# Kernel optimization log

Hardware: AMD Instinct MI355X
Metric: run time of the kernel (lower is better)

## Reference

```python
import jax, jax.numpy as jnp
import numpy as np

B, T, D = 4, 4096, 1024
H, HD = 16, 64
EPS = 1e-6


def setup_inputs() -> dict:
    key = jax.random.key(0)
    ks = jax.random.split(key, 5)
    scale = 1.0 / np.sqrt(D)
    return {
        "x": jax.random.normal(ks[0], (B, T, D), dtype=jnp.float32),
        "Wq": jax.random.normal(ks[1], (D, H * HD), dtype=jnp.float32) * scale,
        "Wk": jax.random.normal(ks[2], (D, H * HD), dtype=jnp.float32) * scale,
        "Wv": jax.random.normal(ks[3], (D, H * HD), dtype=jnp.float32) * scale,
        "Wo": jax.random.normal(ks[4], (H * HD, D), dtype=jnp.float32) * scale,
    }


def _feature_map(x):
    # ELU + 1 feature map (always positive)
    return jax.nn.elu(x) + 1.0


def _causal_linear_attention(q, k, v, eps=EPS):
    # q,k,v: (B,H,T,Dk/Dv) -> scan over T with running state
    Dk = q.shape[-1]
    Dv = v.shape[-1]
    qT = jnp.moveaxis(q, 2, 0)  # (T,B,H,Dk)
    kT = jnp.moveaxis(k, 2, 0)
    vT = jnp.moveaxis(v, 2, 0)

    S0 = jnp.zeros((q.shape[0], q.shape[1], Dk, Dv), dtype=q.dtype)
    z0 = jnp.zeros((q.shape[0], q.shape[1], Dk), dtype=q.dtype)

    def step(carry, qkv_t):
        S, z = carry
        q_t, k_t, v_t = qkv_t
        S = S + jnp.einsum('bhd,bhe->bhde', k_t, v_t)
        z = z + k_t
        num = jnp.einsum('bhd,bhde->bhe', q_t, S)
        den = jnp.einsum('bhd,bhd->bh', q_t, z) + eps
        return (S, z), num / den[..., None]

    _, yT = jax.lax.scan(step, (S0, z0), (qT, kT, vT))  # yT: (T,B,H,Dv)
    return jnp.moveaxis(yT, 0, 2)  # (B,H,T,Dv)


def reference(x, Wq, Wk, Wv, Wo):
    b, t, _ = x.shape

    def proj(W):
        return (x @ W).reshape(b, t, H, HD).transpose(0, 2, 1, 3)  # (B,H,T,HD)

    q = _feature_map(proj(Wq))
    k = _feature_map(proj(Wk))
    v = proj(Wv)
    y = _causal_linear_attention(q, k, v)  # (B,H,T,HD)
    y = y.transpose(0, 2, 1, 3).reshape(b, t, H * HD)
    return y @ Wo
```

## Files before the change

kernel.cpp:

```cpp
#include <hip/hip_runtime.h>


typedef __bf16 bf16;
typedef __bf16 bf16x4 __attribute__((ext_vector_type(4)));
typedef __bf16 bf16x8 __attribute__((ext_vector_type(8)));
typedef float f32x4 __attribute__((ext_vector_type(4)));

#define EPS 1e-6f

#define BAR() asm volatile("s_barrier" ::: "memory")
#define VMCNT4() asm volatile("s_waitcnt vmcnt(4)" ::: "memory")
#define VMCNT0() asm volatile("s_waitcnt vmcnt(0)" ::: "memory")

__device__ __forceinline__ void gl_lds16(const void* g, void* l) {
  __builtin_amdgcn_global_load_lds(
      (__attribute__((address_space(1))) void*)g,
      (__attribute__((address_space(3))) void*)l, 16, 0, 0);
}

__device__ __forceinline__ float fmact(float v) {
  return v > 0.f ? v + 1.f : __expf(v);
}

__global__ __launch_bounds__(256) void cvt_bf16(const float* __restrict__ in,
                                                bf16* __restrict__ out, int n8) {
  int i = blockIdx.x * 256 + threadIdx.x;
  if (i >= n8) return;
  size_t base = (size_t)i * 8;
  float4 v0 = *(const float4*)&in[base];
  float4 v1 = *(const float4*)&in[base + 4];
  bf16x8 o;
  o[0] = (bf16)v0.x; o[1] = (bf16)v0.y; o[2] = (bf16)v0.z; o[3] = (bf16)v0.w;
  o[4] = (bf16)v1.x; o[5] = (bf16)v1.y; o[6] = (bf16)v1.z; o[7] = (bf16)v1.w;
  *(bf16x8*)&out[base] = o;
}

__global__ __launch_bounds__(256) void wtrans(const float* __restrict__ W,
                                              bf16* __restrict__ WT) {
  __shared__ float tile[64][65];
  const int k0 = blockIdx.x * 64, n0 = blockIdx.y * 64;
  const int t = threadIdx.x;
  {
    const int r4 = t / 16, c4 = (t % 16) * 4;
#pragma unroll
    for (int rr = 0; rr < 4; ++rr) {
      int r = r4 + rr * 16;
      float4 v = *(const float4*)&W[(size_t)(k0 + r) * 1024 + n0 + c4];
      tile[r][c4] = v.x; tile[r][c4 + 1] = v.y;
      tile[r][c4 + 2] = v.z; tile[r][c4 + 3] = v.w;
    }
  }
  __syncthreads();
  const int nl = t / 4, kb = (t % 4) * 16;
  bf16x8 o0, o1;
#pragma unroll
  for (int j = 0; j < 8; ++j) {
    o0[j] = (bf16)tile[kb + j][nl];
    o1[j] = (bf16)tile[kb + 8 + j][nl];
  }
  *(bf16x8*)&WT[(size_t)(n0 + nl) * 1024 + k0 + kb] = o0;
  *(bf16x8*)&WT[(size_t)(n0 + nl) * 1024 + k0 + kb + 8] = o1;
}

template <int PROJ>
__global__ __launch_bounds__(512, 2) void gemm8(const bf16* __restrict__ A,
                                                const bf16* __restrict__ BT,
                                                bf16* __restrict__ Obf,
                                                float* __restrict__ Of,
                                                const int N, const int gy) {
  extern __shared__ bf16 lds[];
  const int t = threadIdx.x;
  const int w = t >> 6, l = t & 63;
  const int nwg = (int)gridDim.x, cpx = nwg >> 3;
  const int f = ((int)blockIdx.x & 7) * cpx + ((int)blockIdx.x >> 3);
  const int bx = f / gy, by = f - bx * gy;
  const int m0 = bx * 256, n0 = by * 256;
  const int wm = (w >> 2) * 128, wn = (w & 3) * 64;
  const int lr = l & 15, lg = l >> 4;
  const int aslc = (w >> 2) * 8192;
  const int bslc = 16384 + ((w & 3) >> 1) * 8192;
  const int brow = (w & 1) * 64;
  const int srow = t >> 3;
  const int scol = ((t & 7) ^ ((t >> 3) & 7)) * 8;

  f32x4 acc[8][4] = {};
  bf16x8 bv[8];

#define FRAG(c, slc, sr_, ks_)                                          \
  (*(const bf16x8*)&lds[(c) * 32768 + (slc) + (sr_) * 64 +              \
                        (((ks_) * 32 + lg * 8) ^ (((sr_) & 7) << 3))])

#define STG(dbuf, slc, rbase, PTR, kt)                                        \
  do {                                                                        \
    const bf16* _s = (PTR) + (size_t)((rbase) + srow) * 1024 + (kt) * 64 + scol; \
    bf16* _d = lds + (dbuf) * 32768 + (slc) + w * 512;                        \
    gl_lds16(_s, _d);                                                         \
    gl_lds16(_s + 65536, _d + 4096);                                          \
  } while (0)

#define PHASE(c, q, STAGE_STMT, VM)                                           \
  {                                                                           \
    bf16x8 av[4];                                                             \
    _Pragma("unroll") for (int mi = 0; mi < 2; ++mi)                          \
      _Pragma("unroll") for (int kk = 0; kk < 2; ++kk)                        \
        av[mi * 2 + kk] = FRAG(c, aslc, (q) * 32 + mi * 16 + lr, kk);         \
    if ((q) == 0) {                                                           \
      _Pragma("unroll") for (int n = 0; n < 4; ++n)                           \
        _Pragma("unroll") for (int kk = 0; kk < 2; ++kk)                      \
          bv[n * 2 + kk] = FRAG(c, bslc, brow + n * 16 + lr, kk);             \
    }                                                                         \
    STAGE_STMT;                                                               \
    if (VM) VMCNT4();                                                         \
    BAR();                                                                    \
    __builtin_amdgcn_s_setprio(1);                                            \
    _Pragma("unroll") for (int mi = 0; mi < 2; ++mi)                          \
      _Pragma("unroll") for (int n = 0; n < 4; ++n)                           \
        _Pragma("unroll") for (int kk = 0; kk < 2; ++kk)                      \
          acc[(q) * 2 + mi][n] = __builtin_amdgcn_mfma_f32_16x16x32_bf16(     \
              av[mi * 2 + kk], bv[n * 2 + kk], acc[(q) * 2 + mi][n], 0, 0, 0);\
    __builtin_amdgcn_s_setprio(0);                                            \
    BAR();                                                                    \
  }

  STG(0, 0, m0, A, 0);        STG(0, 8192, m0 + 128, A, 0);
  STG(0, 16384, n0, BT, 0);   STG(0, 24576, n0 + 128, BT, 0);
  STG(1, 16384, n0, BT, 1);   STG(1, 24576, n0 + 128, BT, 1);
  VMCNT4();
  BAR();

#pragma unroll 1
  for (int I = 0; I < 8; ++I) {
    const int t2 = 2 * I;
    const int k1 = t2 + 1;
    const int k2 = (t2 + 2 > 15) ? 15 : t2 + 2;
    const int k3 = (t2 + 3 > 15) ? 15 : t2 + 3;
    PHASE(0, 0, STG(1, 0, m0, A, k1), 0);
    PHASE(0, 1, STG(1, 8192, m0 + 128, A, k1), 0);
    PHASE(0, 2, STG(0, 16384, n0, BT, k2), 0);
    PHASE(0, 3, STG(0, 24576, n0 + 128, BT, k2), 1);
    PHASE(1, 0, STG(0, 0, m0, A, k2), 0);
    PHASE(1, 1, STG(0, 8192, m0 + 128, A, k2), 0);
    PHASE(1, 2, STG(1, 16384, n0, BT, k3), 0);
    PHASE(1, 3, STG(1, 24576, n0 + 128, BT, k3), 1);
  }
  VMCNT0();
#undef PHASE
#undef STG
#undef FRAG
#pragma unroll
  for (int m = 0; m < 8; ++m)
#pragma unroll
    for (int n = 0; n < 4; ++n)
#pragma unroll
      for (int r = 0; r < 4; ++r) {
        int row = m0 + wm + m * 16 + lg * 4 + r;
        int col = n0 + wn + n * 16 + lr;
        float v = acc[m][n][r];
        if (PROJ) {
          if (col < 2048) v = fmact(v);
          Obf[(size_t)row * N + col] = (bf16)v;
        } else {
          Of[(size_t)row * N + col] = v;
        }
      }
}

__global__ __launch_bounds__(256) void chunk_ktv(const bf16* __restrict__ QKV,
                                                 float* __restrict__ S_ws,
                                                 float* __restrict__ z_ws) {
  const int blk = blockIdx.x;
  const int bh = blk >> 5, c = blk & 31;
  const int b = bh >> 4, h = bh & 15;
  const size_t rowbase = (size_t)b * 4096 + (size_t)c * 128;
  __shared__ alignas(16) bf16 KT[64 * 136];
  __shared__ alignas(16) bf16 VT[64 * 136];
  const int t = threadIdx.x;
  {
    const int r = t >> 1, c0 = (t & 1) * 32;
    const bf16* kp = QKV + (rowbase + r) * 3072 + 1024 + h * 64 + c0;
    const bf16* vp = QKV + (rowbase + r) * 3072 + 2048 + h * 64 + c0;
    bf16x8 kv[4], vv[4];
#pragma unroll
    for (int q8 = 0; q8 < 4; ++q8) {
      kv[q8] = *(const bf16x8*)&kp[q8 * 8];
      vv[q8] = *(const bf16x8*)&vp[q8 * 8];
    }
#pragma unroll
    for (int q8 = 0; q8 < 4; ++q8)
#pragma unroll
      for (int j = 0; j < 8; ++j) {
        KT[(c0 + q8 * 8 + j) * 136 + r] = kv[q8][j];
        VT[(c0 + q8 * 8 + j) * 136 + r] = vv[q8][j];
      }
  }
  __syncthreads();
  if (t < 64) {
    float z = 0.f;
    for (int tt = 0; tt < 128; ++tt) z += (float)KT[t * 136 + tt];
    z_ws[(size_t)blk * 64 + t] = z;
  }
  const int l = t & 63, w = t >> 6;
  const int lr = l & 15, lg = l >> 4, lk = lg * 8;
  f32x4 acc[4] = {};
#pragma unroll
  for (int ks = 0; ks < 4; ++ks) {
    const int k0 = ks * 32;
    bf16x8 a = *(const bf16x8*)&VT[(w * 16 + lr) * 136 + k0 + lk];
#pragma unroll
    for (int n = 0; n < 4; ++n) {
      bf16x8 bk = *(const bf16x8*)&KT[(n * 16 + lr) * 136 + k0 + lk];
      acc[n] = __builtin_amdgcn_mfma_f32_16x16x32_bf16(a, bk, acc[n], 0, 0, 0);
    }
  }
#pragma unroll
  for (int n = 0; n < 4; ++n)
#pragma unroll
    for (int r = 0; r < 4; ++r) {
      int e = w * 16 + lg * 4 + r;
      int d = n * 16 + lr;
      S_ws[((size_t)blk * 64 + e) * 64 + d] = acc[n][r];
    }
}

__global__ __launch_bounds__(256) void prefix_scan(const float* __restrict__ S_ws,
                                                   const float* __restrict__ z_ws,
                                                   bf16* __restrict__ STp,
                                                   float* __restrict__ zP) {
  const int bh = blockIdx.x >> 2, dq = blockIdx.x & 3;
  const int t = threadIdx.x;
  const int e = t >> 2, d0 = dq * 16 + (t & 3) * 4;
  float r0 = 0.f, r1 = 0.f, r2 = 0.f, r3 = 0.f, zr = 0.f;
  const bool doz = (dq == 0) && (t < 64);
  for (int c = 0; c < 32; ++c) {
    const size_t cb = (size_t)bh * 32 + c;
    bf16x4 o;
    o[0] = (bf16)r0; o[1] = (bf16)r1; o[2] = (bf16)r2; o[3] = (bf16)r3;
    *(bf16x4*)&STp[cb * 4096 + e * 64 + d0] = o;
    if (doz) {
      zP[cb * 64 + t] = zr;
      zr += z_ws[cb * 64 + t];
    }
    float4 v = *(const float4*)&S_ws[cb * 4096 + e * 64 + d0];
    r0 += v.x; r1 += v.y; r2 += v.z; r3 += v.w;
  }
}

__global__ __launch_bounds__(256) void chunk_attn(const bf16* __restrict__ QKV,
                                                  const bf16* __restrict__ STp,
                                                  const float* __restrict__ zP,
                                                  bf16* __restrict__ Y) {
  const int blk = blockIdx.x;
  const int bh = blk >> 5, c = blk & 31;
  const int b = bh >> 4, h = bh & 15;
  const size_t cb = (size_t)bh * 32 + c;
  const size_t rowbase = (size_t)b * 4096 + (size_t)c * 128;
  const bf16* Q = QKV + rowbase * 3072 + h * 64;
  const bf16* K = QKV + rowbase * 3072 + 1024 + h * 64;
  const bf16* V = QKV + rowbase * 3072 + 2048 + h * 64;
  __shared__ alignas(16) bf16 VT[64 * 136];
  __shared__ alignas(16) bf16 P[128 * 136];
  __shared__ float den[128];
  const int t = threadIdx.x;
  {
    const int r = t >> 1, c0 = (t & 1) * 32;
    const bf16* vp = V + (size_t)r * 3072 + c0;
    bf16x8 vv[4];
#pragma unroll
    for (int q8 = 0; q8 < 4; ++q8) vv[q8] = *(const bf16x8*)&vp[q8 * 8];
#pragma unroll
    for (int q8 = 0; q8 < 4; ++q8)
#pragma unroll
      for (int j = 0; j < 8; ++j) VT[(c0 + q8 * 8 + j) * 136 + r] = vv[q8][j];
  }
  const int l = t & 63, w = t >> 6;
  const int lr = l & 15, lg = l >> 4, lk = lg * 8;
  f32x4 acc[2][4] = {};
  f32x4 accs[2][8] = {};
#pragma unroll
  for (int kq = 0; kq < 2; ++kq) {
    const int k0 = kq * 32;
    bf16x8 am[2];
#pragma unroll
    for (int m = 0; m < 2; ++m)
      am[m] = *(const bf16x8*)&Q[(size_t)(w * 32 + m * 16 + lr) * 3072 + k0 + lk];
#pragma unroll
    for (int n = 0; n < 4; ++n) {
      bf16x8 bs = *(const bf16x8*)&STp[cb * 4096 + (size_t)(n * 16 + lr) * 64 + k0 + lk];
#pragma unroll
      for (int m = 0; m < 2; ++m)
        acc[m][n] = __builtin_amdgcn_mfma_f32_16x16x32_bf16(am[m], bs, acc[m][n], 0, 0, 0);
    }
#pragma unroll
    for (int n = 0; n < 8; ++n) {
      bf16x8 bk = *(const bf16x8*)&K[(size_t)(n * 16 + lr) * 3072 + k0 + lk];
#pragma unroll
      for (int m = 0; m < 2; ++m)
        accs[m][n] = __builtin_amdgcn_mfma_f32_16x16x32_bf16(am[m], bk, accs[m][n], 0, 0, 0);
    }
  }
#pragma unroll
  for (int m = 0; m < 2; ++m)
#pragma unroll
    for (int r = 0; r < 4; ++r) {
      const int row_c = w * 32 + m * 16 + lg * 4 + r;
      float s = 0.f;
#pragma unroll
      for (int n = 0; n < 8; ++n) {
        const int col_c = n * 16 + lr;
        float v = accs[m][n][r];
        v = (col_c <= row_c) ? v : 0.f;
        accs[m][n][r] = v;
        s += v;
      }
      s += __shfl_xor(s, 1);
      s += __shfl_xor(s, 2);
      s += __shfl_xor(s, 4);
      s += __shfl_xor(s, 8);
      if (lr == 0) den[row_c] = s;
#pragma unroll
      for (int n = 0; n < 8; ++n)
        P[row_c * 136 + n * 16 + lr] = (bf16)accs[m][n][r];
    }
  __syncthreads();
  if (t < 128) {
    float s = EPS;
    const bf16* qr = Q + (size_t)t * 3072;
    const float* zp = zP + cb * 64;
#pragma unroll
    for (int d8 = 0; d8 < 64; d8 += 8) {
      bf16x8 qv = *(const bf16x8*)&qr[d8];
#pragma unroll
      for (int j = 0; j < 8; ++j) s += (float)qv[j] * zp[d8 + j];
    }
    den[t] += s;
  }
#pragma unroll
  for (int ks = 0; ks < 4; ++ks) {
    const int k0 = ks * 32;
    bf16x8 ap[2];
#pragma unroll
    for (int m = 0; m < 2; ++m)
      ap[m] = *(const bf16x8*)&P[(w * 32 + m * 16 + lr) * 136 + k0 + lk];
#pragma unroll
    for (int n = 0; n < 4; ++n) {
      bf16x8 bv = *(const bf16x8*)&VT[(n * 16 + lr) * 136 + k0 + lk];
#pragma unroll
      for (int m = 0; m < 2; ++m)
        acc[m][n] = __builtin_amdgcn_mfma_f32_16x16x32_bf16(ap[m], bv, acc[m][n], 0, 0, 0);
    }
  }
  __syncthreads();
#pragma unroll
  for (int m = 0; m < 2; ++m)
#pragma unroll
    for (int n = 0; n < 4; ++n)
#pragma unroll
      for (int r = 0; r < 4; ++r) {
        const int row_c = w * 32 + m * 16 + lg * 4 + r;
        const int col = n * 16 + lr;
        float y = acc[m][n][r] / den[row_c];
        Y[(rowbase + row_c) * 1024 + h * 64 + col] = (bf16)y;
      }
}

extern "C" void kernel_launch(void* const* d_in, const int* in_sizes, int n_in,
                              void* d_out, int out_size, void* d_ws, size_t ws_size,
                              hipStream_t stream) {
  (void)in_sizes; (void)n_in; (void)out_size; (void)ws_size;
  const float* x  = (const float*)d_in[0];
  const float* Wq = (const float*)d_in[1];
  const float* Wk = (const float*)d_in[2];
  const float* Wv = (const float*)d_in[3];
  const float* Wo = (const float*)d_in[4];
  char* ws = (char*)d_ws;
  bf16*  XB   = (bf16*)ws;
  bf16*  WT3  = (bf16*)(ws + 33554432);
  bf16*  WOT  = (bf16*)(ws + 39845888);
  bf16*  QKV  = (bf16*)(ws + 41943040);
  float* S_ws = (float*)(ws + 142606336);
  float* z_ws = (float*)(ws + 176160768);
  bf16*  STp  = (bf16*)(ws + 176685056);
  float* zP   = (float*)(ws + 193462272);
  bf16*  Y    = XB;

  {
    auto k1 = gemm8<1>; auto k0 = gemm8<0>;
    (void)hipFuncSetAttribute((const void*)k1,
        hipFuncAttributeMaxDynamicSharedMemorySize, 131072);
    (void)hipFuncSetAttribute((const void*)k0,
        hipFuncAttributeMaxDynamicSharedMemorySize, 131072);
  }

  cvt_bf16<<<8192, 256, 0, stream>>>(x, XB, 2097152);
  wtrans<<<dim3(16, 16), 256, 0, stream>>>(Wq, WT3);
  wtrans<<<dim3(16, 16), 256, 0, stream>>>(Wk, WT3 + 1048576);
  wtrans<<<dim3(16, 16), 256, 0, stream>>>(Wv, WT3 + 2097152);
  wtrans<<<dim3(16, 16), 256, 0, stream>>>(Wo, WOT);
  gemm8<1><<<768, 512, 131072, stream>>>(XB, WT3, QKV, nullptr, 3072, 12);
  chunk_ktv<<<2048, 256, 0, stream>>>(QKV, S_ws, z_ws);
  prefix_scan<<<256, 256, 0, stream>>>(S_ws, z_ws, STp, zP);
  chunk_attn<<<2048, 256, 0, stream>>>(QKV, STp, zP, Y);
  gemm8<0><<<256, 512, 131072, stream>>>(Y, WOT, nullptr, (float*)d_out, 1024, 4);
}
```

Measured before the change: 275.7 us.

## Switch GEMM to 32x32x16 MFMA tiles and prefetch prefix-scan loads

The bf16 GEMM moves from 16x16x32 MFMA instructions to 32x32x16, which changes the LDS fragment indexing, the split of work across phases, the accumulator layout and the epilogue index mapping. The larger MFMA tile needs fewer LDS fragment reads per flop and fewer instructions issued. The prefix_scan kernel also software-pipelines its global loads by fetching chunk c+1 while chunk c is accumulated, to hide memory latency on its serial loop. In exchange the GEMM takes on more register pressure, and the reworked fragment and output mappings have to be exactly right.

```diff
diff --git a/kernel.cpp b/kernel.cpp
--- a/kernel.cpp
+++ b/kernel.cpp
@@ -5,6 +5,7 @@
 typedef __bf16 bf16x4 __attribute__((ext_vector_type(4)));
 typedef __bf16 bf16x8 __attribute__((ext_vector_type(8)));
 typedef float f32x4 __attribute__((ext_vector_type(4)));
+typedef float f32x16 __attribute__((ext_vector_type(16)));
 
 #define EPS 1e-6f
 
@@ -76,19 +77,19 @@
   const int bx = f / gy, by = f - bx * gy;
   const int m0 = bx * 256, n0 = by * 256;
   const int wm = (w >> 2) * 128, wn = (w & 3) * 64;
-  const int lr = l & 15, lg = l >> 4;
+  const int l31 = l & 31, lh = l >> 5;
   const int aslc = (w >> 2) * 8192;
   const int bslc = 16384 + ((w & 3) >> 1) * 8192;
   const int brow = (w & 1) * 64;
   const int srow = t >> 3;
   const int scol = ((t & 7) ^ ((t >> 3) & 7)) * 8;
 
-  f32x4 acc[8][4] = {};
+  f32x16 acc[4][2] = {};
   bf16x8 bv[8];
 
-#define FRAG(c, slc, sr_, ks_)                                          \
+#define FRAG32(c, slc, sr_, ks_)                                        \
   (*(const bf16x8*)&lds[(c) * 32768 + (slc) + (sr_) * 64 +              \
-                        (((ks_) * 32 + lg * 8) ^ (((sr_) & 7) << 3))])
+                        (((ks_) * 16 + lh * 8) ^ (((sr_) & 7) << 3))])
 
 #define STG(dbuf, slc, rbase, PTR, kt)                                        \
   do {                                                                        \
@@ -98,26 +99,29 @@
     gl_lds16(_s + 65536, _d + 4096);                                          \
   } while (0)
 
-#define PHASE(c, q, STAGE_STMT, VM)                                           \
+#define PHASE32(c, mp, kh, dobv, bvkh, STAGE_STMT, VM)                        \
   {                                                                           \
     bf16x8 av[4];                                                             \
     _Pragma("unroll") for (int mi = 0; mi < 2; ++mi)                          \
       _Pragma("unroll") for (int kk = 0; kk < 2; ++kk)                        \
-        av[mi * 2 + kk] = FRAG(c, aslc, (q) * 32 + mi * 16 + lr, kk);         \
-    if ((q) == 0) {                                                           \
-      _Pragma("unroll") for (int n = 0; n < 4; ++n)                           \
+        av[mi * 2 + kk] =                                                     \
+            FRAG32(c, aslc, ((mp) * 2 + mi) * 32 + l31, (kh) * 2 + kk);       \
+    if (dobv) {                                                               \
+      _Pragma("unroll") for (int nt = 0; nt < 2; ++nt)                        \
         _Pragma("unroll") for (int kk = 0; kk < 2; ++kk)                      \
-          bv[n * 2 + kk] = FRAG(c, bslc, brow + n * 16 + lr, kk);             \
+          bv[nt * 4 + (bvkh) * 2 + kk] =                                      \
+              FRAG32(c, bslc, brow + nt * 32 + l31, (bvkh) * 2 + kk);         \
     }                                                                         \
     STAGE_STMT;                                                               \
     if (VM) VMCNT4();                                                         \
     BAR();                                                                    \
     __builtin_amdgcn_s_setprio(1);                                            \
-    _Pragma("unroll") for (int mi = 0; mi < 2; ++mi)                          \
-      _Pragma("unroll") for (int n = 0; n < 4; ++n)                           \
-        _Pragma("unroll") for (int kk = 0; kk < 2; ++kk)                      \
-          acc[(q) * 2 + mi][n] = __builtin_amdgcn_mfma_f32_16x16x32_bf16(     \
-              av[mi * 2 + kk], bv[n * 2 + kk], acc[(q) * 2 + mi][n], 0, 0, 0);\
+    _Pragma("unroll") for (int kk = 0; kk < 2; ++kk)                          \
+      _Pragma("unroll") for (int mi = 0; mi < 2; ++mi)                        \
+        _Pragma("unroll") for (int nt = 0; nt < 2; ++nt)                      \
+          acc[(mp) * 2 + mi][nt] = __builtin_amdgcn_mfma_f32_32x32x16_bf16(   \
+              av[mi * 2 + kk], bv[nt * 4 + (kh) * 2 + kk],                    \
+              acc[(mp) * 2 + mi][nt], 0, 0, 0);                               \
     __builtin_amdgcn_s_setprio(0);                                            \
     BAR();                                                                    \
   }
@@ -134,28 +138,28 @@
     const int k1 = t2 + 1;
     const int k2 = (t2 + 2 > 15) ? 15 : t2 + 2;
     const int k3 = (t2 + 3 > 15) ? 15 : t2 + 3;
-    PHASE(0, 0, STG(1, 0, m0, A, k1), 0);
-    PHASE(0, 1, STG(1, 8192, m0 + 128, A, k1), 0);
-    PHASE(0, 2, STG(0, 16384, n0, BT, k2), 0);
-    PHASE(0, 3, STG(0, 24576, n0 + 128, BT, k2), 1);
-    PHASE(1, 0, STG(0, 0, m0, A, k2), 0);
-    PHASE(1, 1, STG(0, 8192, m0 + 128, A, k2), 0);
-    PHASE(1, 2, STG(1, 16384, n0, BT, k3), 0);
-    PHASE(1, 3, STG(1, 24576, n0 + 128, BT, k3), 1);
+    PHASE32(0, 0, 0, 1, 0, STG(1, 0, m0, A, k1), 0);
+    PHASE32(0, 1, 0, 1, 1, STG(1, 8192, m0 + 128, A, k1), 0);
+    PHASE32(0, 0, 1, 0, 0, STG(0, 16384, n0, BT, k2), 0);
+    PHASE32(0, 1, 1, 0, 0, STG(0, 24576, n0 + 128, BT, k2), 1);
+    PHASE32(1, 0, 0, 1, 0, STG(0, 0, m0, A, k2), 0);
+    PHASE32(1, 1, 0, 1, 1, STG(0, 8192, m0 + 128, A, k2), 0);
+    PHASE32(1, 0, 1, 0, 0, STG(1, 16384, n0, BT, k3), 0);
+    PHASE32(1, 1, 1, 0, 0, STG(1, 24576, n0 + 128, BT, k3), 1);
   }
   VMCNT0();
-#undef PHASE
+#undef PHASE32
 #undef STG
-#undef FRAG
-#pragma unroll
-  for (int m = 0; m < 8; ++m)
-#pragma unroll
-    for (int n = 0; n < 4; ++n)
-#pragma unroll
-      for (int r = 0; r < 4; ++r) {
-        int row = m0 + wm + m * 16 + lg * 4 + r;
-        int col = n0 + wn + n * 16 + lr;
-        float v = acc[m][n][r];
+#undef FRAG32
+#pragma unroll
+  for (int q = 0; q < 4; ++q)
+#pragma unroll
+    for (int nt = 0; nt < 2; ++nt)
+#pragma unroll
+      for (int rg = 0; rg < 16; ++rg) {
+        int row = m0 + wm + q * 32 + (rg & 3) + 8 * (rg >> 2) + 4 * lh;
+        int col = n0 + wn + nt * 32 + l31;
+        float v = acc[q][nt][rg];
         if (PROJ) {
           if (col < 2048) v = fmact(v);
           Obf[(size_t)row * N + col] = (bf16)v;
@@ -231,17 +235,24 @@
   const int e = t >> 2, d0 = dq * 16 + (t & 3) * 4;
   float r0 = 0.f, r1 = 0.f, r2 = 0.f, r3 = 0.f, zr = 0.f;
   const bool doz = (dq == 0) && (t < 64);
+  const size_t base = (size_t)bh * 32;
+  float4 v = *(const float4*)&S_ws[base * 4096 + e * 64 + d0];
+  float zv = doz ? z_ws[base * 64 + t] : 0.f;
   for (int c = 0; c < 32; ++c) {
-    const size_t cb = (size_t)bh * 32 + c;
+    float4 vn = {0.f, 0.f, 0.f, 0.f};
+    float zn = 0.f;
+    if (c < 31) {
+      vn = *(const float4*)&S_ws[(base + c + 1) * 4096 + e * 64 + d0];
+      if (doz) zn = z_ws[(base + c + 1) * 64 + t];
+    }
+    const size_t cb = base + c;
     bf16x4 o;
     o[0] = (bf16)r0; o[1] = (bf16)r1; o[2] = (bf16)r2; o[3] = (bf16)r3;
     *(bf16x4*)&STp[cb * 4096 + e * 64 + d0] = o;
-    if (doz) {
-      zP[cb * 64 + t] = zr;
-      zr += z_ws[cb * 64 + t];
-    }
-    float4 v = *(const float4*)&S_ws[cb * 4096 + e * 64 + d0];
+    if (doz) zP[cb * 64 + t] = zr;
     r0 += v.x; r1 += v.y; r2 += v.z; r3 += v.w;
+    zr += zv;
+    v = vn; zv = zn;
   }
 }
 
```

Measured after the change: 287.2 us. 1.04x slower.

## Fuse prep kernels, parallelize chunk z-sum, and prefetch in prefix scan

Applied to the files above, without the earlier changes.

Merges the x-to-bf16 conversion and the four weight transposes into one prep launch, cutting four kernel launches and the gaps between them. In chunk_ktv the per-chunk key sum, previously done serially by 64 threads, is split across all 256 threads with a shared-memory reduction, at the cost of one extra barrier. In prefix_scan the next chunk's S and z values are loaded one iteration ahead, so global load latency overlaps the running-sum arithmetic. Each piece is small, and the kernels they touch are short next to the GEMMs.

```diff
diff --git a/kernel.cpp b/kernel.cpp
--- a/kernel.cpp
+++ b/kernel.cpp
@@ -22,24 +22,32 @@
   return v > 0.f ? v + 1.f : __expf(v);
 }
 
-__global__ __launch_bounds__(256) void cvt_bf16(const float* __restrict__ in,
-                                                bf16* __restrict__ out, int n8) {
-  int i = blockIdx.x * 256 + threadIdx.x;
-  if (i >= n8) return;
-  size_t base = (size_t)i * 8;
-  float4 v0 = *(const float4*)&in[base];
-  float4 v1 = *(const float4*)&in[base + 4];
-  bf16x8 o;
-  o[0] = (bf16)v0.x; o[1] = (bf16)v0.y; o[2] = (bf16)v0.z; o[3] = (bf16)v0.w;
-  o[4] = (bf16)v1.x; o[5] = (bf16)v1.y; o[6] = (bf16)v1.z; o[7] = (bf16)v1.w;
-  *(bf16x8*)&out[base] = o;
-}
-
-__global__ __launch_bounds__(256) void wtrans(const float* __restrict__ W,
-                                              bf16* __restrict__ WT) {
+__global__ __launch_bounds__(256) void prep(const float* __restrict__ x,
+                                            const float* __restrict__ Wq,
+                                            const float* __restrict__ Wk,
+                                            const float* __restrict__ Wv,
+                                            const float* __restrict__ Wo,
+                                            bf16* __restrict__ XB,
+                                            bf16* __restrict__ WT3,
+                                            bf16* __restrict__ WOT) {
+  const int bid = blockIdx.x;
+  const int t = threadIdx.x;
+  if (bid < 8192) {
+    size_t base = ((size_t)bid * 256 + t) * 8;
+    float4 v0 = *(const float4*)&x[base];
+    float4 v1 = *(const float4*)&x[base + 4];
+    bf16x8 o;
+    o[0] = (bf16)v0.x; o[1] = (bf16)v0.y; o[2] = (bf16)v0.z; o[3] = (bf16)v0.w;
+    o[4] = (bf16)v1.x; o[5] = (bf16)v1.y; o[6] = (bf16)v1.z; o[7] = (bf16)v1.w;
+    *(bf16x8*)&XB[base] = o;
+    return;
+  }
   __shared__ float tile[64][65];
-  const int k0 = blockIdx.x * 64, n0 = blockIdx.y * 64;
-  const int t = threadIdx.x;
+  const int wi = (bid - 8192) >> 8;
+  const int local = (bid - 8192) & 255;
+  const float* W = (wi == 0) ? Wq : (wi == 1) ? Wk : (wi == 2) ? Wv : Wo;
+  bf16* WT = (wi == 3) ? WOT : WT3 + (size_t)wi * 1048576;
+  const int k0 = (local & 15) * 64, n0 = (local >> 4) * 64;
   {
     const int r4 = t / 16, c4 = (t % 16) * 4;
 #pragma unroll
@@ -174,6 +182,7 @@
   const size_t rowbase = (size_t)b * 4096 + (size_t)c * 128;
   __shared__ alignas(16) bf16 KT[64 * 136];
   __shared__ alignas(16) bf16 VT[64 * 136];
+  __shared__ float zpart[4][64];
   const int t = threadIdx.x;
   {
     const int r = t >> 1, c0 = (t & 1) * 32;
@@ -194,11 +203,17 @@
       }
   }
   __syncthreads();
-  if (t < 64) {
-    float z = 0.f;
-    for (int tt = 0; tt < 128; ++tt) z += (float)KT[t * 136 + tt];
-    z_ws[(size_t)blk * 64 + t] = z;
-  }
+  {
+    const int d = t & 63, part = t >> 6;
+    float zs = 0.f;
+#pragma unroll
+    for (int tt = 0; tt < 32; ++tt) zs += (float)KT[d * 136 + part * 32 + tt];
+    zpart[part][d] = zs;
+  }
+  __syncthreads();
+  if (t < 64)
+    z_ws[(size_t)blk * 64 + t] =
+        zpart[0][t] + zpart[1][t] + zpart[2][t] + zpart[3][t];
   const int l = t & 63, w = t >> 6;
   const int lr = l & 15, lg = l >> 4, lk = lg * 8;
   f32x4 acc[4] = {};
@@ -231,17 +246,24 @@
   const int e = t >> 2, d0 = dq * 16 + (t & 3) * 4;
   float r0 = 0.f, r1 = 0.f, r2 = 0.f, r3 = 0.f, zr = 0.f;
   const bool doz = (dq == 0) && (t < 64);
+  const size_t base = (size_t)bh * 32;
+  float4 v = *(const float4*)&S_ws[base * 4096 + e * 64 + d0];
+  float zv = doz ? z_ws[base * 64 + t] : 0.f;
   for (int c = 0; c < 32; ++c) {
-    const size_t cb = (size_t)bh * 32 + c;
+    float4 vn = {0.f, 0.f, 0.f, 0.f};
+    float zn = 0.f;
+    if (c < 31) {
+      vn = *(const float4*)&S_ws[(base + c + 1) * 4096 + e * 64 + d0];
+      if (doz) zn = z_ws[(base + c + 1) * 64 + t];
+    }
+    const size_t cb = base + c;
     bf16x4 o;
     o[0] = (bf16)r0; o[1] = (bf16)r1; o[2] = (bf16)r2; o[3] = (bf16)r3;
     *(bf16x4*)&STp[cb * 4096 + e * 64 + d0] = o;
-    if (doz) {
-      zP[cb * 64 + t] = zr;
-      zr += z_ws[cb * 64 + t];
-    }
-    float4 v = *(const float4*)&S_ws[cb * 4096 + e * 64 + d0];
+    if (doz) zP[cb * 64 + t] = zr;
     r0 += v.x; r1 += v.y; r2 += v.z; r3 += v.w;
+    zr += zv;
+    v = vn; zv = zn;
   }
 }
 
@@ -391,11 +413,7 @@
         hipFuncAttributeMaxDynamicSharedMemorySize, 131072);
   }
 
-  cvt_bf16<<<8192, 256, 0, stream>>>(x, XB, 2097152);
-  wtrans<<<dim3(16, 16), 256, 0, stream>>>(Wq, WT3);
-  wtrans<<<dim3(16, 16), 256, 0, stream>>>(Wk, WT3 + 1048576);
-  wtrans<<<dim3(16, 16), 256, 0, stream>>>(Wv, WT3 + 2097152);
-  wtrans<<<dim3(16, 16), 256, 0, stream>>>(Wo, WOT);
+  prep<<<9216, 256, 0, stream>>>(x, Wq, Wk, Wv, Wo, XB, WT3, WOT);
   gemm8<1><<<768, 512, 131072, stream>>>(XB, WT3, QKV, nullptr, 3072, 12);
   chunk_ktv<<<2048, 256, 0, stream>>>(QKV, S_ws, z_ws);
   prefix_scan<<<256, 256, 0, stream>>>(S_ws, z_ws, STp, zP);
```

Measured after the change: 265.0 us. 1.04x faster.
